# Kernel tuning notes

Measured on AMD Instinct MI355X. Metric: run time of the kernel, lower is better.

The kernel has to match this reference:

```python
import jax, jax.numpy as jnp
import numpy as np

N_HEAD = 16
MASKED_BIAS = -10000.0


def setup_inputs() -> dict:
    key = jax.random.key(0)
    k1, k2, k3 = jax.random.split(key, 3)
    B, T, E = 2, 2048, 1024
    return {
        "stacked": jax.random.normal(k1, (B, T, E), dtype=jnp.float32),
        "w_attn": jax.random.normal(k2, (E, 3 * E), dtype=jnp.float32) * 0.02,
        "b_attn": jnp.zeros((3 * E,), dtype=jnp.float32),
        "w_proj": jax.random.normal(k3, (E, E), dtype=jnp.float32) * 0.02,
        "b_proj": jnp.zeros((E,), dtype=jnp.float32),
    }


def reference(stacked, w_attn, b_attn, w_proj, b_proj):
    B, T, E = stacked.shape
    nh = N_HEAD
    dh = E // nh
    # Conv1D (GPT-2): x @ W + b
    qkv = stacked @ w_attn + b_attn            # (B, T, 3E)
    q, k, v = jnp.split(qkv, 3, axis=-1)
    q = q.reshape(B, T, nh, dh).transpose(0, 2, 1, 3)  # (B, nh, T, dh)
    k = k.reshape(B, T, nh, dh).transpose(0, 2, 1, 3)
    v = v.reshape(B, T, nh, dh).transpose(0, 2, 1, 3)
    # scores = Q @ K^T / sqrt(dh)
    w = jnp.einsum("bhtd,bhsd->bhts", q, k) / jnp.sqrt(jnp.float32(dh))
    causal = jnp.tril(jnp.ones((T, T), dtype=bool))
    w = jnp.where(causal, w, jnp.float32(MASKED_BIAS))
    w = jax.nn.softmax(w, axis=-1)
    out = jnp.einsum("bhts,bhsd->bhtd", w, v)  # (B, nh, T, dh)
    out = out.transpose(0, 2, 1, 3).reshape(B, T, E)
    attn_z = out @ w_proj + b_proj
    return attn_z
```

## Files before the change

kernel.cpp:

```cpp
#include <hip/hip_runtime.h>
#include <hip/hip_bf16.h>

#define B_ 2
#define T_ 2048
#define E_ 1024
#define NH 16
#define M_ (B_*T_)
#define N3E 3072

typedef __attribute__((ext_vector_type(8))) short short8;
typedef __attribute__((ext_vector_type(4))) float f32x4;

__device__ __forceinline__ unsigned short f2bf(float f) {
  unsigned u = __builtin_bit_cast(unsigned, f);
  unsigned r = 0x7FFFu + ((u >> 16) & 1u);
  return (unsigned short)((u + r) >> 16);
}

__device__ __forceinline__ float bf2f(unsigned short s) {
  return __builtin_bit_cast(float, ((unsigned)s) << 16);
}

__device__ __forceinline__ unsigned cvtpk(float a, float b) {
  unsigned r;
  asm("v_cvt_pk_bf16_f32 %0, %1, %2" : "=v"(r) : "v"(a), "v"(b));
  return r;
}

__device__ __forceinline__ float exp2fast(float x) {
  float r;
  asm("v_exp_f32 %0, %1" : "=v"(r) : "v"(x));
  return r;
}

__device__ __forceinline__ void gload16(const void* g, void* l) {
  __builtin_amdgcn_global_load_lds(
      (const __attribute__((address_space(1))) unsigned int*)g,
      (__attribute__((address_space(3))) unsigned int*)l, 16, 0, 0);
}

__global__ void cast_kernel(const float* __restrict__ in,
                            unsigned short* __restrict__ out, int n8) {
  int i = blockIdx.x * blockDim.x + threadIdx.x;
  if (i >= n8) return;
  const float4* p = (const float4*)in + (size_t)i * 2;
  float4 a = p[0], b = p[1];
  short8 o;
  o[0] = (short)f2bf(a.x); o[1] = (short)f2bf(a.y);
  o[2] = (short)f2bf(a.z); o[3] = (short)f2bf(a.w);
  o[4] = (short)f2bf(b.x); o[5] = (short)f2bf(b.y);
  o[6] = (short)f2bf(b.z); o[7] = (short)f2bf(b.w);
  *(short8*)(out + (size_t)i * 8) = o;
}

__global__ void transpose_cast(const float* __restrict__ in,
                               unsigned short* __restrict__ out, int R, int C) {
  __shared__ float tile[32][33];
  int c0 = blockIdx.x * 32, r0 = blockIdx.y * 32;
  int tx = threadIdx.x & 31, ty = threadIdx.x >> 5;
#pragma unroll
  for (int i = 0; i < 4; i++) {
    int r = ty + i * 8;
    tile[r][tx] = in[(size_t)(r0 + r) * C + c0 + tx];
  }
  __syncthreads();
#pragma unroll
  for (int i = 0; i < 4; i++) {
    int r = ty + i * 8;
    out[(size_t)(c0 + r) * R + r0 + tx] = f2bf(tile[tx][r]);
  }
}

template <int OUTF32>
__global__ __launch_bounds__(256) void gemm_bt(
    const unsigned short* __restrict__ A, const unsigned short* __restrict__ Bt,
    const float* __restrict__ bias, void* __restrict__ outp,
    int M, int N, int K) {
  __shared__ __attribute__((aligned(16))) unsigned short Asm[128 * 32];
  __shared__ __attribute__((aligned(16))) unsigned short Bsm[128 * 32];
  const int tid = threadIdx.x;
  const int lane = tid & 63;
  const int wid = tid >> 6;
  const int wr = wid >> 1, wc = wid & 1;
  const int li = lane & 15, g = lane >> 4;
  const int bm = blockIdx.y * 128, bn = blockIdx.x * 128;

  f32x4 acc[4][4] = {};

  const int srow = tid >> 2;
  const int scol = (tid & 3) * 8;
  const unsigned short* Ag = A + (size_t)(bm + srow) * K + scol;
  const unsigned short* Bg = Bt + (size_t)(bn + srow) * K + scol;
  char* AsmB = (char*)Asm;
  char* BsmB = (char*)Bsm;
  const int ldsoff = tid * 16;

  for (int k0 = 0; k0 < K; k0 += 32) {
    __syncthreads();
    gload16(Ag + k0, AsmB + ldsoff);
    gload16(Ag + (size_t)64 * K + k0, AsmB + ldsoff + 4096);
    gload16(Bg + k0, BsmB + ldsoff);
    gload16(Bg + (size_t)64 * K + k0, BsmB + ldsoff + 4096);
    __syncthreads();
    short8 af[4], bf[4];
#pragma unroll
    for (int i = 0; i < 4; i++)
      af[i] = *(const short8*)&Asm[(wr * 64 + i * 16 + li) * 32 + g * 8];
#pragma unroll
    for (int j = 0; j < 4; j++)
      bf[j] = *(const short8*)&Bsm[(wc * 64 + j * 16 + li) * 32 + g * 8];
#pragma unroll
    for (int i = 0; i < 4; i++)
#pragma unroll
      for (int j = 0; j < 4; j++)
        acc[i][j] = __builtin_amdgcn_mfma_f32_16x16x32_bf16(af[i], bf[j],
                                                            acc[i][j], 0, 0, 0);
  }

#pragma unroll
  for (int j = 0; j < 4; j++) {
    int col = bn + wc * 64 + j * 16 + li;
    float bs = bias[col];
#pragma unroll
    for (int i = 0; i < 4; i++) {
      int row0 = bm + wr * 64 + i * 16 + g * 4;
#pragma unroll
      for (int r = 0; r < 4; r++) {
        float v = acc[i][j][r] + bs;
        if (OUTF32)
          ((float*)outp)[(size_t)(row0 + r) * N + col] = v;
        else
          ((unsigned short*)outp)[(size_t)(row0 + r) * N + col] = f2bf(v);
      }
    }
  }
}

__device__ __forceinline__ f32x4 mfma16(short8 a, short8 b, f32x4 c) {
  return __builtin_amdgcn_mfma_f32_16x16x32_bf16(a, b, c, 0, 0, 0);
}

__device__ __forceinline__ void attn_tile(
    const unsigned short* Ksm, const unsigned short* Vts,
    unsigned short (*PsmW)[64], short8 qf0, short8 qf1,
    float& m2, float& l2, f32x4* O, int qrel, bool diag, int li, int g) {
  f32x4 S[4];
  __builtin_amdgcn_s_setprio(1);
#pragma unroll
  for (int ct = 0; ct < 4; ct++) {
    int r = ct * 16 + li;
    int sw = r & 7;
    short8 k0f = *(const short8*)&Ksm[r * 64 + ((g ^ sw) << 3)];
    short8 k1f = *(const short8*)&Ksm[r * 64 + (((g + 4) ^ sw) << 3)];
    f32x4 z = {0.f, 0.f, 0.f, 0.f};
    z = mfma16(k0f, qf0, z);
    z = mfma16(k1f, qf1, z);
    S[ct] = z;
  }
  __builtin_amdgcn_s_setprio(0);

  if (diag) {
#pragma unroll
    for (int ct = 0; ct < 4; ct++)
#pragma unroll
      for (int r = 0; r < 4; r++)
        if (ct * 16 + g * 4 + r > qrel) S[ct][r] = -30000.f;
  }

  float tmax = S[0][0];
#pragma unroll
  for (int ct = 0; ct < 4; ct++)
#pragma unroll
    for (int r = 0; r < 4; r++) tmax = fmaxf(tmax, S[ct][r]);
  tmax = fmaxf(tmax, __shfl_xor(tmax, 16));
  tmax = fmaxf(tmax, __shfl_xor(tmax, 32));

  if (__any(tmax > m2 + 11.5f)) {
    float mn = fmaxf(m2, tmax);
    float cs = exp2fast(m2 - mn);
    l2 *= cs;
#pragma unroll
    for (int c2 = 0; c2 < 4; c2++)
#pragma unroll
      for (int r = 0; r < 4; r++) O[c2][r] *= cs;
    m2 = mn;
  }

  float rsum = 0.f;
#pragma unroll
  for (int ct = 0; ct < 4; ct++) {
    float p0 = exp2fast(S[ct][0] - m2);
    float p1 = exp2fast(S[ct][1] - m2);
    float p2 = exp2fast(S[ct][2] - m2);
    float p3 = exp2fast(S[ct][3] - m2);
    rsum += (p0 + p1) + (p2 + p3);
    uint2 pk;
    pk.x = cvtpk(p0, p1);
    pk.y = cvtpk(p2, p3);
    int pc = (2 * ct + (g >> 1)) ^ (li & 7);
    *(uint2*)&PsmW[li][pc * 8 + (g & 1) * 4] = pk;
  }
  rsum += __shfl_xor(rsum, 16);
  rsum += __shfl_xor(rsum, 32);
  l2 += rsum;

  __builtin_amdgcn_s_setprio(1);
#pragma unroll
  for (int kk = 0; kk < 2; kk++) {
    short8 pf = *(const short8*)&PsmW[li][((4 * kk + g) ^ (li & 7)) * 8];
#pragma unroll
    for (int c2 = 0; c2 < 4; c2++) {
      int d = c2 * 16 + li;
      int swd = ((d >> 3) ^ d) & 7;
      short8 vf = *(const short8*)&Vts[d * 64 + (((kk * 4 + g) ^ swd) << 3)];
      O[c2] = mfma16(vf, pf, O[c2]);
    }
  }
  __builtin_amdgcn_s_setprio(0);
}

__global__ __launch_bounds__(256) void attn_kernel(
    const unsigned short* __restrict__ qkv, unsigned short* __restrict__ aout) {
  const int pair = blockIdx.x;
  const int h = blockIdx.y, b = blockIdx.z;
  const int qa = pair, qb = (T_ / 64 - 1) - pair;
  const int tid = threadIdx.x, lane = tid & 63, w = tid >> 6;
  const int li = lane & 15, g = lane >> 4;

  __shared__ __attribute__((aligned(16))) unsigned short Ksm[2][64 * 64];
  __shared__ __attribute__((aligned(16))) unsigned short Vts[2][64 * 64];
  __shared__ __attribute__((aligned(16))) unsigned short Psm[4][16][64];

  const size_t rs = 3 * E_;
  const unsigned short* base = qkv + (size_t)b * T_ * rs + h * 64;
  const unsigned short* Kg = base + E_;
  const unsigned short* Vg = base + 2 * E_;

  const float QSC = 0.18033688f;
  short8 qfa0, qfa1, qfb0, qfb1;
  {
    const unsigned short* qrow = base + (size_t)(qa * 64 + w * 16 + li) * rs;
    short8 v0 = *(const short8*)(qrow + g * 8);
    short8 v1 = *(const short8*)(qrow + 32 + g * 8);
    qrow = base + (size_t)(qb * 64 + w * 16 + li) * rs;
    short8 v2 = *(const short8*)(qrow + g * 8);
    short8 v3 = *(const short8*)(qrow + 32 + g * 8);
#pragma unroll
    for (int j = 0; j < 8; j++) {
      qfa0[j] = (short)f2bf(bf2f((unsigned short)v0[j]) * QSC);
      qfa1[j] = (short)f2bf(bf2f((unsigned short)v1[j]) * QSC);
      qfb0[j] = (short)f2bf(bf2f((unsigned short)v2[j]) * QSC);
      qfb1[j] = (short)f2bf(bf2f((unsigned short)v3[j]) * QSC);
    }
  }

  float ma = -1e30f, la = 0.f, mb = -1e30f, lb = 0.f;
  f32x4 Oa[4] = {}, Ob[4] = {};

  short8 vreg[2];

#pragma unroll
  for (int p = 0; p < 2; p++) {
    int idx = tid + p * 256;
    int r = idx >> 3, ch = idx & 7;
    int sc = (ch ^ (r & 7)) * 8;
    gload16(Kg + (size_t)r * rs + sc, (char*)&Ksm[0][0] + idx * 16);
  }
#pragma unroll
  for (int p = 0; p < 2; p++) {
    int idx = tid + p * 256;
    int r = idx >> 3, c = (idx & 7) * 8;
    vreg[p] = *(const short8*)(Vg + (size_t)r * rs + c);
  }
#pragma unroll
  for (int p = 0; p < 2; p++) {
    int idx = tid + p * 256;
    int r = idx >> 3, ch = idx & 7;
#pragma unroll
    for (int j = 0; j < 8; j++) {
      int d = ch * 8 + j;
      Vts[0][(d * 64 + r) ^ (((ch ^ j) & 7) << 3)] = (unsigned short)vreg[p][j];
    }
  }
  asm volatile("s_waitcnt vmcnt(0)" ::: "memory");
  __syncthreads();

  const int nt = qb + 1;
  for (int kv = 0; kv < nt; kv++) {
    const int cur = kv & 1, nxt = cur ^ 1;
    const bool pre = (kv + 1 < nt);
    if (pre) {
      const int s1 = (kv + 1) * 64;
#pragma unroll
      for (int p = 0; p < 2; p++) {
        int idx = tid + p * 256;
        int r = idx >> 3, c = (idx & 7) * 8;
        vreg[p] = *(const short8*)(Vg + (size_t)(s1 + r) * rs + c);
      }
#pragma unroll
      for (int p = 0; p < 2; p++) {
        int idx = tid + p * 256;
        int r = idx >> 3, ch = idx & 7;
        int sc = (ch ^ (r & 7)) * 8;
        gload16(Kg + (size_t)(s1 + r) * rs + sc,
                (char*)&Ksm[nxt][0] + idx * 16);
      }
    }

    attn_tile(&Ksm[cur][0], &Vts[cur][0], Psm[w], qfb0, qfb1, mb, lb, Ob,
              qb * 64 + w * 16 + li - kv * 64, kv == qb, li, g);
    if (kv <= qa)
      attn_tile(&Ksm[cur][0], &Vts[cur][0], Psm[w], qfa0, qfa1, ma, la, Oa,
                qa * 64 + w * 16 + li - kv * 64, kv == qa, li, g);

    if (pre) {
#pragma unroll
      for (int p = 0; p < 2; p++) {
        int idx = tid + p * 256;
        int r = idx >> 3, ch = idx & 7;
#pragma unroll
        for (int j = 0; j < 8; j++) {
          int d = ch * 8 + j;
          Vts[nxt][(d * 64 + r) ^ (((ch ^ j) & 7) << 3)] =
              (unsigned short)vreg[p][j];
        }
      }
    }
    asm volatile("s_waitcnt vmcnt(0)" ::: "memory");
    __syncthreads();
  }

  const float inva = 1.f / la, invb = 1.f / lb;
  const int rowa = b * T_ + qa * 64 + w * 16 + li;
  const int rowb = b * T_ + qb * 64 + w * 16 + li;
#pragma unroll
  for (int c2 = 0; c2 < 4; c2++) {
    uint2 oa, ob;
    oa.x = cvtpk(Oa[c2][0] * inva, Oa[c2][1] * inva);
    oa.y = cvtpk(Oa[c2][2] * inva, Oa[c2][3] * inva);
    ob.x = cvtpk(Ob[c2][0] * invb, Ob[c2][1] * invb);
    ob.y = cvtpk(Ob[c2][2] * invb, Ob[c2][3] * invb);
    *(uint2*)&aout[(size_t)rowa * E_ + h * 64 + c2 * 16 + g * 4] = oa;
    *(uint2*)&aout[(size_t)rowb * E_ + h * 64 + c2 * 16 + g * 4] = ob;
  }
}

extern "C" void kernel_launch(void* const* d_in, const int* in_sizes, int n_in,
                              void* d_out, int out_size, void* d_ws,
                              size_t ws_size, hipStream_t stream) {
  const float* stacked = (const float*)d_in[0];
  const float* w_attn = (const float*)d_in[1];
  const float* b_attn = (const float*)d_in[2];
  const float* w_proj = (const float*)d_in[3];
  const float* b_proj = (const float*)d_in[4];
  float* out = (float*)d_out;

  unsigned short* Abf = (unsigned short*)d_ws;
  unsigned short* WaT = Abf + (size_t)M_ * E_;
  unsigned short* WpT = WaT + (size_t)N3E * E_;
  unsigned short* qkv = WpT + (size_t)E_ * E_;
  unsigned short* aout = qkv + (size_t)M_ * N3E;

  cast_kernel<<<(M_ * E_ / 8 + 255) / 256, 256, 0, stream>>>(stacked, Abf,
                                                             M_ * E_ / 8);
  transpose_cast<<<dim3(N3E / 32, E_ / 32), 256, 0, stream>>>(w_attn, WaT, E_,
                                                              N3E);
  transpose_cast<<<dim3(E_ / 32, E_ / 32), 256, 0, stream>>>(w_proj, WpT, E_,
                                                             E_);
  gemm_bt<0><<<dim3(N3E / 128, M_ / 128), 256, 0, stream>>>(Abf, WaT, b_attn,
                                                            qkv, M_, N3E, E_);
  attn_kernel<<<dim3(T_ / 128, NH, B_), 256, 0, stream>>>(qkv, aout);
  gemm_bt<1><<<dim3(E_ / 128, M_ / 128), 256, 0, stream>>>(aout, WpT, b_proj,
                                                           out, M_, E_, E_);
}
```

Measured before the change: 130.5 us.

## Pre-transpose V in a separate kernel and load it asynchronously into attention

Adds a kernel that transposes the V part of the QKV buffer into a per-batch [E, T] layout in workspace. The attention kernel then fetches V tiles with the same direct global-to-LDS async loads used for K, with a matching swizzle, instead of register loads followed by scalar scattered LDS stores inside the loop. This removes per-iteration transpose work and LDS store traffic from the hot loop. The cost is an extra kernel launch, an extra pass over V in memory, and more workspace.

```diff
diff --git a/kernel.cpp b/kernel.cpp
--- a/kernel.cpp
+++ b/kernel.cpp
@@ -68,6 +68,33 @@
   for (int i = 0; i < 4; i++) {
     int r = ty + i * 8;
     out[(size_t)(c0 + r) * R + r0 + tx] = f2bf(tile[tx][r]);
+  }
+}
+
+__global__ __launch_bounds__(256) void vtrans_kernel(
+    const unsigned short* __restrict__ qkv, unsigned short* __restrict__ Vt) {
+  const int s0 = blockIdx.x * 64;
+  const int c0 = blockIdx.y * 64;
+  const int b = blockIdx.z;
+  __shared__ unsigned short t[64][72];
+  const int tid = threadIdx.x;
+  const size_t rs = 3 * E_;
+  const unsigned short* src = qkv + (size_t)(b * T_) * rs + 2 * E_;
+#pragma unroll
+  for (int p = 0; p < 2; p++) {
+    int idx = tid + p * 256;
+    int r = idx >> 3, c = (idx & 7) * 8;
+    *(short8*)&t[r][c] = *(const short8*)(src + (size_t)(s0 + r) * rs + c0 + c);
+  }
+  __syncthreads();
+#pragma unroll
+  for (int p = 0; p < 2; p++) {
+    int idx = tid + p * 256;
+    int dr = idx >> 3, sc = (idx & 7) * 8;
+    short8 o;
+#pragma unroll
+    for (int j = 0; j < 8; j++) o[j] = (short)t[sc + j][dr];
+    *(short8*)&Vt[(size_t)(b * E_ + c0 + dr) * T_ + s0 + sc] = o;
   }
 }
 
@@ -211,8 +238,7 @@
 #pragma unroll
     for (int c2 = 0; c2 < 4; c2++) {
       int d = c2 * 16 + li;
-      int swd = ((d >> 3) ^ d) & 7;
-      short8 vf = *(const short8*)&Vts[d * 64 + (((kk * 4 + g) ^ swd) << 3)];
+      short8 vf = *(const short8*)&Vts[d * 64 + (((kk * 4 + g) ^ (li & 7)) << 3)];
       O[c2] = mfma16(vf, pf, O[c2]);
     }
   }
@@ -220,7 +246,8 @@
 }
 
 __global__ __launch_bounds__(256) void attn_kernel(
-    const unsigned short* __restrict__ qkv, unsigned short* __restrict__ aout) {
+    const unsigned short* __restrict__ qkv, const unsigned short* __restrict__ Vt,
+    unsigned short* __restrict__ aout) {
   const int pair = blockIdx.x;
   const int h = blockIdx.y, b = blockIdx.z;
   const int qa = pair, qb = (T_ / 64 - 1) - pair;
@@ -234,7 +261,7 @@
   const size_t rs = 3 * E_;
   const unsigned short* base = qkv + (size_t)b * T_ * rs + h * 64;
   const unsigned short* Kg = base + E_;
-  const unsigned short* Vg = base + 2 * E_;
+  const unsigned short* Vtg = Vt + (size_t)(b * E_ + h * 64) * T_;
 
   const float QSC = 0.18033688f;
   short8 qfa0, qfa1, qfb0, qfb1;
@@ -257,30 +284,13 @@
   float ma = -1e30f, la = 0.f, mb = -1e30f, lb = 0.f;
   f32x4 Oa[4] = {}, Ob[4] = {};
 
-  short8 vreg[2];
-
 #pragma unroll
   for (int p = 0; p < 2; p++) {
     int idx = tid + p * 256;
     int r = idx >> 3, ch = idx & 7;
     int sc = (ch ^ (r & 7)) * 8;
     gload16(Kg + (size_t)r * rs + sc, (char*)&Ksm[0][0] + idx * 16);
-  }
-#pragma unroll
-  for (int p = 0; p < 2; p++) {
-    int idx = tid + p * 256;
-    int r = idx >> 3, c = (idx & 7) * 8;
-    vreg[p] = *(const short8*)(Vg + (size_t)r * rs + c);
-  }
-#pragma unroll
-  for (int p = 0; p < 2; p++) {
-    int idx = tid + p * 256;
-    int r = idx >> 3, ch = idx & 7;
-#pragma unroll
-    for (int j = 0; j < 8; j++) {
-      int d = ch * 8 + j;
-      Vts[0][(d * 64 + r) ^ (((ch ^ j) & 7) << 3)] = (unsigned short)vreg[p][j];
-    }
+    gload16(Vtg + (size_t)r * T_ + sc, (char*)&Vts[0][0] + idx * 16);
   }
   asm volatile("s_waitcnt vmcnt(0)" ::: "memory");
   __syncthreads();
@@ -294,16 +304,12 @@
 #pragma unroll
       for (int p = 0; p < 2; p++) {
         int idx = tid + p * 256;
-        int r = idx >> 3, c = (idx & 7) * 8;
-        vreg[p] = *(const short8*)(Vg + (size_t)(s1 + r) * rs + c);
-      }
-#pragma unroll
-      for (int p = 0; p < 2; p++) {
-        int idx = tid + p * 256;
         int r = idx >> 3, ch = idx & 7;
         int sc = (ch ^ (r & 7)) * 8;
         gload16(Kg + (size_t)(s1 + r) * rs + sc,
                 (char*)&Ksm[nxt][0] + idx * 16);
+        gload16(Vtg + (size_t)r * T_ + s1 + sc,
+                (char*)&Vts[nxt][0] + idx * 16);
       }
     }
 
@@ -313,19 +319,6 @@
       attn_tile(&Ksm[cur][0], &Vts[cur][0], Psm[w], qfa0, qfa1, ma, la, Oa,
                 qa * 64 + w * 16 + li - kv * 64, kv == qa, li, g);
 
-    if (pre) {
-#pragma unroll
-      for (int p = 0; p < 2; p++) {
-        int idx = tid + p * 256;
-        int r = idx >> 3, ch = idx & 7;
-#pragma unroll
-        for (int j = 0; j < 8; j++) {
-          int d = ch * 8 + j;
-          Vts[nxt][(d * 64 + r) ^ (((ch ^ j) & 7) << 3)] =
-              (unsigned short)vreg[p][j];
-        }
-      }
-    }
     asm volatile("s_waitcnt vmcnt(0)" ::: "memory");
     __syncthreads();
   }
@@ -360,6 +353,7 @@
   unsigned short* WpT = WaT + (size_t)N3E * E_;
   unsigned short* qkv = WpT + (size_t)E_ * E_;
   unsigned short* aout = qkv + (size_t)M_ * N3E;
+  unsigned short* Vt = aout + (size_t)M_ * E_;
 
   cast_kernel<<<(M_ * E_ / 8 + 255) / 256, 256, 0, stream>>>(stacked, Abf,
                                                              M_ * E_ / 8);
@@ -369,7 +363,8 @@
                                                              E_);
   gemm_bt<0><<<dim3(N3E / 128, M_ / 128), 256, 0, stream>>>(Abf, WaT, b_attn,
                                                             qkv, M_, N3E, E_);
-  attn_kernel<<<dim3(T_ / 128, NH, B_), 256, 0, stream>>>(qkv, aout);
+  vtrans_kernel<<<dim3(T_ / 64, E_ / 64, B_), 256, 0, stream>>>(qkv, Vt);
+  attn_kernel<<<dim3(T_ / 128, NH, B_), 256, 0, stream>>>(qkv, Vt, aout);
   gemm_bt<1><<<dim3(E_ / 128, M_ / 128), 256, 0, stream>>>(aout, WpT, b_proj,
                                                            out, M_, E_, E_);
 }
```

New measurement: 130.0 us. No clear change (-0.4%).
